# Optimization experiments

Hardware: AMD Instinct MI355X
Metric: run time of the kernel (lower is better)

## Reference

```python
import jax, jax.numpy as jnp
import numpy as np

B, N, C, H = 2, 2048, 1024, 16
D = C // H  # head_dim = 64

def setup_inputs() -> dict:
    key = jax.random.key(0)
    ks = jax.random.split(key, 8)
    x = jax.random.normal(ks[0], (B, N, C), jnp.float32)
    mask = jax.random.uniform(ks[1], (H, N, N), jnp.float32)
    gamma = jax.random.uniform(ks[2], (H,), jnp.float32)  # per-head decay in (0,1)
    state_prev = jax.random.normal(ks[3], (B, H, D, D), jnp.float32)
    w_scale = 0.02
    W_qkv = jax.random.normal(ks[4], (C, 3 * C), jnp.float32) * w_scale
    b_qkv = jnp.zeros((3 * C,), jnp.float32)
    W_out = jax.random.normal(ks[5], (C, C), jnp.float32) * w_scale
    b_out = jnp.zeros((C,), jnp.float32)
    return dict(x=x, mask=mask, gamma=gamma, state_prev=state_prev,
                W_qkv=W_qkv, b_qkv=b_qkv, W_out=W_out, b_out=b_out)

def reference(x, mask, gamma, state_prev, W_qkv, b_qkv, W_out, b_out):
    # Retention.chunkwise with state_prev (mode='chunkwise')
    b, n, c = x.shape
    h = gamma.shape[0]
    d = c // h
    scale = d ** -0.5
    qkv = (x @ W_qkv + b_qkv).reshape(b, n, 3, h, d)
    q = qkv[:, :, 0].transpose(0, 2, 1, 3) * scale  # [B,H,N,D]
    k = qkv[:, :, 1].transpose(0, 2, 1, 3)
    v = qkv[:, :, 2].transpose(0, 2, 1, 3)
    # intra-chunk decay-masked retention: [B,H,N,N]
    ret = jnp.einsum('bhnd,bhmd->bhnm', q, k) * mask
    ret = jnp.einsum('bhnm,bhmd->bhnd', ret, v)  # [B,H,N,D]
    inner_pos = jnp.arange(1, n + 1, dtype=x.dtype)  # [N], 1-based positions
    # state = sum_n gamma^(N-n) * k_n^T v_n (no [B,H,N,D,D] materialization)
    state_decays = gamma[:, None] ** (n - inner_pos)[None, :]  # [H,N]
    state = jnp.einsum('bhnd,bhne,hn->bhde', k, v, state_decays)  # [B,H,D,D]
    chunk_decay = gamma ** n  # [H]
    state = state + state_prev * chunk_decay[None, :, None, None]
    # cross-chunk retention against previous state
    cross = jnp.einsum('bhnd,bhde->bhne', q, state_prev)
    cross = cross * (gamma[None, :, None, None] ** inner_pos[None, None, :, None])
    ret = (ret + cross).transpose(0, 2, 1, 3).reshape(b, n, c)
    out = ret @ W_out + b_out
    return (out, state)
```

## Files before the change

### kernel.cpp

```cpp
#include <hip/hip_runtime.h>
#include <hip/hip_bf16.h>
#include <cstdint>

#define DI __device__ __forceinline__

typedef __attribute__((ext_vector_type(8))) short v8s;
typedef __attribute__((ext_vector_type(4))) float v4f;

constexpr int Bc = 2, Nc = 2048, Cc = 1024, Hc = 16, Dc = 64;

DI float bfbits(uint32_t u) { union { uint32_t i; float f; } c; c.i = u; return c.f; }
DI unsigned short f2bf(float f) {
    union { float f; uint32_t u; } c; c.f = f;
    uint32_t r = c.u + 0x7FFFu + ((c.u >> 16) & 1u);
    return (unsigned short)(r >> 16);
}
DI void unpackb8(uint4 u, float* f) {
    f[0] = bfbits(u.x << 16); f[1] = bfbits(u.x & 0xFFFF0000u);
    f[2] = bfbits(u.y << 16); f[3] = bfbits(u.y & 0xFFFF0000u);
    f[4] = bfbits(u.z << 16); f[5] = bfbits(u.z & 0xFFFF0000u);
    f[6] = bfbits(u.w << 16); f[7] = bfbits(u.w & 0xFFFF0000u);
}
DI float gpow(float g, float p) {
    if (p <= 0.f) return 1.f;
    if (g <= 0.f) return 0.f;
    return exp2f(p * log2f(g));
}

__global__ __launch_bounds__(256) void cvt_bf16(
    const float* __restrict__ in, unsigned short* __restrict__ out, int n8)
{
    int i = blockIdx.x * 256 + threadIdx.x;
    if (i >= n8) return;
    float4 a = ((const float4*)in)[i * 2];
    float4 b = ((const float4*)in)[i * 2 + 1];
    ushort4 r0; r0.x = f2bf(a.x); r0.y = f2bf(a.y); r0.z = f2bf(a.z); r0.w = f2bf(a.w);
    ushort4 r1; r1.x = f2bf(b.x); r1.y = f2bf(b.y); r1.z = f2bf(b.z); r1.w = f2bf(b.w);
    ((ushort4*)out)[i * 2] = r0; ((ushort4*)out)[i * 2 + 1] = r1;
}

__global__ __launch_bounds__(256) void transpose_cvt(
    const float* __restrict__ in, unsigned short* __restrict__ out, int R, int C)
{
    __shared__ float T[64][65];
    const int tid = threadIdx.x;
    const int r0 = blockIdx.y * 64, c0 = blockIdx.x * 64;
    #pragma unroll
    for (int rep = 0; rep < 4; rep++) {
        int row = (tid >> 4) + rep * 16, col = (tid & 15) * 4;
        float4 v = *reinterpret_cast<const float4*>(in + (size_t)(r0 + row) * C + c0 + col);
        T[row][col] = v.x; T[row][col + 1] = v.y; T[row][col + 2] = v.z; T[row][col + 3] = v.w;
    }
    __syncthreads();
    #pragma unroll
    for (int rep = 0; rep < 4; rep++) {
        int ocr = (tid >> 4) + rep * 16, j4 = (tid & 15) * 4;
        ushort4 w;
        w.x = f2bf(T[j4][ocr]);     w.y = f2bf(T[j4 + 1][ocr]);
        w.z = f2bf(T[j4 + 2][ocr]); w.w = f2bf(T[j4 + 3][ocr]);
        *reinterpret_cast<ushort4*>(out + (size_t)(c0 + ocr) * R + r0 + j4) = w;
    }
}

__global__ __launch_bounds__(256) void transpose_v(
    const unsigned short* __restrict__ in, unsigned short* __restrict__ out)
{
    __shared__ unsigned short T[64][72];
    const int tid = threadIdx.x;
    const int n0 = blockIdx.x * 64;
    const int bh = blockIdx.y;
    const unsigned short* src = in + ((size_t)bh * Nc + n0) * Dc;
    #pragma unroll
    for (int rep = 0; rep < 2; rep++) {
        int r = (tid >> 3) + rep * 32, c = (tid & 7) * 8;
        *(uint4*)&T[r][c] = *(const uint4*)(src + (size_t)r * Dc + c);
    }
    __syncthreads();
    unsigned short* dst = out + (size_t)bh * Dc * Nc + n0;
    #pragma unroll
    for (int rep = 0; rep < 2; rep++) {
        int d = (tid >> 3) + rep * 32, c0 = (tid & 7) * 8;
        union { uint4 u; unsigned short s[8]; } w;
        #pragma unroll
        for (int j = 0; j < 8; j++) w.s[j] = T[c0 + j][d];
        *(uint4*)(dst + (size_t)d * Nc + c0) = w.u;
    }
}

__global__ __launch_bounds__(256) void qkv_mfma(
    const unsigned short* __restrict__ A, const unsigned short* __restrict__ Bt,
    const float* __restrict__ bias,
    unsigned short* __restrict__ q, unsigned short* __restrict__ k,
    unsigned short* __restrict__ v)
{
    __shared__ unsigned short As[128][72];
    __shared__ unsigned short Bs[128][72];
    const int tid = threadIdx.x, wave = tid >> 6, lane = tid & 63;
    const int L = lane & 15, quad = lane >> 4;
    const int wr = (wave >> 1) * 64, wc = (wave & 1) * 64;
    const int row0 = blockIdx.y * 128, col0 = blockIdx.x * 128;
    v4f acc[4][4];
    #pragma unroll
    for (int i = 0; i < 4; i++)
        #pragma unroll
        for (int j = 0; j < 4; j++) { acc[i][j][0]=0.f; acc[i][j][1]=0.f; acc[i][j][2]=0.f; acc[i][j][3]=0.f; }
    for (int k0 = 0; k0 < 1024; k0 += 64) {
        __syncthreads();
        #pragma unroll
        for (int rep = 0; rep < 4; rep++) {
            int r = (tid >> 3) + rep * 32, cg = (tid & 7) * 8;
            *(uint4*)&As[r][cg] = *(const uint4*)(A  + (size_t)(row0 + r) * 1024 + k0 + cg);
            *(uint4*)&Bs[r][cg] = *(const uint4*)(Bt + (size_t)(col0 + r) * 1024 + k0 + cg);
        }
        __syncthreads();
        #pragma unroll
        for (int half = 0; half < 2; half++) {
            v8s af[4], bf[4];
            #pragma unroll
            for (int s = 0; s < 4; s++) {
                af[s] = *(v8s*)&As[wr + s * 16 + L][half * 32 + quad * 8];
                bf[s] = *(v8s*)&Bs[wc + s * 16 + L][half * 32 + quad * 8];
            }
            #pragma unroll
            for (int i = 0; i < 4; i++)
                #pragma unroll
                for (int j = 0; j < 4; j++)
                    acc[i][j] = __builtin_amdgcn_mfma_f32_16x16x32_bf16(af[i], bf[j], acc[i][j], 0, 0, 0);
        }
    }
    const int which = col0 >> 10;
    #pragma unroll
    for (int j = 0; j < 4; j++) {
        int c = col0 + wc + j * 16 + L;
        int h = (c & 1023) >> 6, d = c & 63;
        float bv = bias[c];
        #pragma unroll
        for (int i = 0; i < 4; i++) {
            #pragma unroll
            for (int reg = 0; reg < 4; reg++) {
                int rr = row0 + wr + i * 16 + quad * 4 + reg;
                int b = rr >> 11, n = rr & 2047;
                float val = acc[i][j][reg] + bv;
                size_t base = (((size_t)(b * Hc + h)) * Nc + n) * Dc + d;
                if (which == 0)      q[base] = f2bf(val * 0.125f);
                else if (which == 1) k[base] = f2bf(val);
                else                 v[base] = f2bf(val);
            }
        }
    }
}

__global__ __launch_bounds__(256) void retention_mfma(
    const unsigned short* __restrict__ qb, const unsigned short* __restrict__ kb,
    const unsigned short* __restrict__ vtb,
    const float* __restrict__ mask, const float* __restrict__ gamma,
    const float* __restrict__ sprev,
    unsigned short* __restrict__ retb, float* __restrict__ pf0, float* __restrict__ pf1)
{
    __shared__ unsigned short K0[64][72], K1[64][72];
    __shared__ unsigned short V0[64][72], V1[64][72];
    __shared__ unsigned short Sm[64][72];
    const int tid = threadIdx.x, wave = tid >> 6, lane = tid & 63;
    const int L = lane & 15, quad = lane >> 4;
    const int h = blockIdx.y;
    const int n0 = blockIdx.x * 64;
    const int chunk = blockIdx.z;
    const int m_base = chunk * 1024;
    const float g = gamma[h];
    const int bh0 = h, bh1 = Hc + h;

    {
        #pragma unroll
        for (int rep = 0; rep < 2; rep++) {
            int r = (tid >> 3) + rep * 32, ch = (tid & 7) * 8;
            *(uint4*)&V0[r][ch] = *(const uint4*)(qb + ((size_t)bh0 * Nc + n0 + r) * Dc + ch);
            *(uint4*)&V1[r][ch] = *(const uint4*)(qb + ((size_t)bh1 * Nc + n0 + r) * Dc + ch);
        }
        if (chunk == 0) {
            int dd = tid >> 2, e0 = (tid & 3) * 16;
            const float* sp0 = sprev + ((size_t)bh0 * 64 + dd) * 64 + e0;
            const float* sp1 = sprev + ((size_t)bh1 * 64 + dd) * 64 + e0;
            #pragma unroll
            for (int j = 0; j < 16; j++) K0[e0 + j][dd] = f2bf(sp0[j]);
            #pragma unroll
            for (int j = 0; j < 16; j++) K1[e0 + j][dd] = f2bf(sp1[j]);
        }
    }
    __syncthreads();
    v8s qf[2][2];
    qf[0][0] = *(v8s*)&V0[wave * 16 + L][quad * 8];
    qf[0][1] = *(v8s*)&V0[wave * 16 + L][32 + quad * 8];
    qf[1][0] = *(v8s*)&V1[wave * 16 + L][quad * 8];
    qf[1][1] = *(v8s*)&V1[wave * 16 + L][32 + quad * 8];
    v4f oacc[2][4];
    if (chunk == 0) {
        #pragma unroll
        for (int b = 0; b < 2; b++) {
            unsigned short (*Kb)[72] = b ? K1 : K0;
            #pragma unroll
            for (int s = 0; s < 4; s++) {
                v4f a; a[0] = 0.f; a[1] = 0.f; a[2] = 0.f; a[3] = 0.f;
                a = __builtin_amdgcn_mfma_f32_16x16x32_bf16(qf[b][0], *(v8s*)&Kb[s * 16 + L][quad * 8], a, 0, 0, 0);
                a = __builtin_amdgcn_mfma_f32_16x16x32_bf16(qf[b][1], *(v8s*)&Kb[s * 16 + L][32 + quad * 8], a, 0, 0, 0);
                oacc[b][s] = a;
            }
        }
        float cf = gpow(g, (float)(n0 + wave * 16 + quad * 4 + 1));
        #pragma unroll
        for (int reg = 0; reg < 4; reg++) {
            #pragma unroll
            for (int b = 0; b < 2; b++)
                #pragma unroll
                for (int s = 0; s < 4; s++) oacc[b][s][reg] *= cf;
            cf *= g;
        }
    } else {
        #pragma unroll
        for (int b = 0; b < 2; b++)
            #pragma unroll
            for (int s = 0; s < 4; s++) { oacc[b][s][0]=0.f; oacc[b][s][1]=0.f; oacc[b][s][2]=0.f; oacc[b][s][3]=0.f; }
    }

    const unsigned short* kp0 = kb + (size_t)bh0 * Nc * Dc;
    const unsigned short* kp1 = kb + (size_t)bh1 * Nc * Dc;
    const unsigned short* vt0 = vtb + (size_t)bh0 * Dc * Nc;
    const unsigned short* vt1 = vtb + (size_t)bh1 * Dc * Nc;
    const float* mbase = mask + (size_t)h * Nc * Nc;

    for (int it = 0; it < 16; ++it) {
        const int m0 = m_base + it * 64;
        __syncthreads();
        {
            #pragma unroll
            for (int rep = 0; rep < 2; rep++) {
                int r = (tid >> 3) + rep * 32, ch = (tid & 7) * 8;
                *(uint4*)&K0[r][ch] = *(const uint4*)(kp0 + (size_t)(m0 + r) * Dc + ch);
                *(uint4*)&K1[r][ch] = *(const uint4*)(kp1 + (size_t)(m0 + r) * Dc + ch);
                *(uint4*)&V0[r][ch] = *(const uint4*)(vt0 + (size_t)r * Nc + m0 + ch);
                *(uint4*)&V1[r][ch] = *(const uint4*)(vt1 + (size_t)r * Nc + m0 + ch);
            }
        }
        __syncthreads();
        float mv[4][4];
        #pragma unroll
        for (int s = 0; s < 4; s++)
            #pragma unroll
            for (int reg = 0; reg < 4; reg++)
                mv[s][reg] = mbase[(size_t)(n0 + wave * 16 + quad * 4 + reg) * Nc + m0 + s * 16 + L];
        #pragma unroll
        for (int b = 0; b < 2; b++) {
            unsigned short (*Kb)[72] = b ? K1 : K0;
            unsigned short (*Vb)[72] = b ? V1 : V0;
            v4f sa[4];
            #pragma unroll
            for (int s = 0; s < 4; s++) {
                v4f a; a[0] = 0.f; a[1] = 0.f; a[2] = 0.f; a[3] = 0.f;
                a = __builtin_amdgcn_mfma_f32_16x16x32_bf16(qf[b][0], *(v8s*)&Kb[s * 16 + L][quad * 8], a, 0, 0, 0);
                a = __builtin_amdgcn_mfma_f32_16x16x32_bf16(qf[b][1], *(v8s*)&Kb[s * 16 + L][32 + quad * 8], a, 0, 0, 0);
                sa[s] = a;
            }
            #pragma unroll
            for (int s = 0; s < 4; s++)
                #pragma unroll
                for (int reg = 0; reg < 4; reg++)
                    Sm[wave * 16 + quad * 4 + reg][s * 16 + L] = f2bf(sa[s][reg] * mv[s][reg]);
            v8s af0 = *(v8s*)&Sm[wave * 16 + L][quad * 8];
            v8s af1 = *(v8s*)&Sm[wave * 16 + L][32 + quad * 8];
            #pragma unroll
            for (int s = 0; s < 4; s++) {
                oacc[b][s] = __builtin_amdgcn_mfma_f32_16x16x32_bf16(af0, *(v8s*)&Vb[s * 16 + L][quad * 8], oacc[b][s], 0, 0, 0);
                oacc[b][s] = __builtin_amdgcn_mfma_f32_16x16x32_bf16(af1, *(v8s*)&Vb[s * 16 + L][32 + quad * 8], oacc[b][s], 0, 0, 0);
            }
        }
    }
    if (chunk == 0) {
        #pragma unroll
        for (int b = 0; b < 2; b++)
            #pragma unroll
            for (int s = 0; s < 4; s++)
                #pragma unroll
                for (int reg = 0; reg < 4; reg++) {
                    int n = n0 + wave * 16 + quad * 4 + reg;
                    retb[((size_t)b * Nc + n) * Cc + h * 64 + s * 16 + L] = f2bf(oacc[b][s][reg]);
                }
    } else {
        #pragma unroll
        for (int b = 0; b < 2; b++) {
            float* pd = b ? pf1 : pf0;
            #pragma unroll
            for (int s = 0; s < 4; s++)
                #pragma unroll
                for (int reg = 0; reg < 4; reg++) {
                    int n = n0 + wave * 16 + quad * 4 + reg;
                    pd[(size_t)n * Cc + h * 64 + s * 16 + L] = oacc[b][s][reg];
                }
        }
    }
}

__global__ __launch_bounds__(256) void add_partial(
    unsigned short* __restrict__ retb,
    const float* __restrict__ pf0, const float* __restrict__ pf1, int n8)
{
    int i = blockIdx.x * 256 + threadIdx.x;
    if (i >= n8) return;
    int e = i * 8;
    const float* pf = (e & (1 << 21)) ? pf1 : pf0;
    const float4* pp = (const float4*)(pf + (e & ((1 << 21) - 1)));
    uint4 a = ((const uint4*)retb)[i];
    float fa[8]; unpackb8(a, fa);
    float4 x0 = pp[0], x1 = pp[1];
    ushort4 r0, r1;
    r0.x = f2bf(fa[0] + x0.x); r0.y = f2bf(fa[1] + x0.y);
    r0.z = f2bf(fa[2] + x0.z); r0.w = f2bf(fa[3] + x0.w);
    r1.x = f2bf(fa[4] + x1.x); r1.y = f2bf(fa[5] + x1.y);
    r1.z = f2bf(fa[6] + x1.z); r1.w = f2bf(fa[7] + x1.w);
    ((ushort4*)retb)[2 * i] = r0; ((ushort4*)retb)[2 * i + 1] = r1;
}

__global__ __launch_bounds__(256) void state_partial(
    const unsigned short* __restrict__ kg, const unsigned short* __restrict__ vg,
    const float* __restrict__ gamma,
    float* __restrict__ partial)
{
    __shared__ float Ks[64][65];
    __shared__ float Vs[64][65];
    __shared__ float wdec[64];
    const int chunk = blockIdx.x;
    const int bh = blockIdx.y;
    const int h = bh & 15;
    const int tid = threadIdx.x;
    const int d = tid >> 2;
    const int e0 = (tid & 3) * 16;
    const float g = gamma[h];
    const unsigned short* kbp = kg + (size_t)bh * Nc * Dc;
    const unsigned short* vbp = vg + (size_t)bh * Nc * Dc;
    float acc[16] = {};
    const int nStart = chunk * 256;
    for (int m0 = nStart; m0 < nStart + 256; m0 += 64) {
        __syncthreads();
        {
            uint4 u0 = *(const uint4*)(kbp + (size_t)(m0 + d) * 64 + e0);
            uint4 u1 = *(const uint4*)(kbp + (size_t)(m0 + d) * 64 + e0 + 8);
            float f[8];
            unpackb8(u0, f);
            #pragma unroll
            for (int j = 0; j < 8; j++) Ks[d][e0 + j] = f[j];
            unpackb8(u1, f);
            #pragma unroll
            for (int j = 0; j < 8; j++) Ks[d][e0 + 8 + j] = f[j];
            uint4 w0 = *(const uint4*)(vbp + (size_t)(m0 + d) * 64 + e0);
            uint4 w1 = *(const uint4*)(vbp + (size_t)(m0 + d) * 64 + e0 + 8);
            unpackb8(w0, f);
            #pragma unroll
            for (int j = 0; j < 8; j++) Vs[d][e0 + j] = f[j];
            unpackb8(w1, f);
            #pragma unroll
            for (int j = 0; j < 8; j++) Vs[d][e0 + 8 + j] = f[j];
        }
        if (tid < 64) wdec[tid] = gpow(g, (float)(2047 - (m0 + tid)));
        __syncthreads();
        for (int nn = 0; nn < 64; nn++) {
            float kw = Ks[nn][d] * wdec[nn];
            #pragma unroll
            for (int j = 0; j < 16; j++) acc[j] += kw * Vs[nn][e0 + j];
        }
    }
    float* pp = partial + (size_t)chunk * (Bc * Hc * Dc * Dc)
              + ((size_t)bh * 64 + d) * 64 + e0;
    #pragma unroll
    for (int j = 0; j < 16; j++) pp[j] = acc[j];
}

__global__ __launch_bounds__(256) void state_reduce(
    const float* __restrict__ partial,
    const float* __restrict__ sprev,
    const float* __restrict__ gamma,
    float* __restrict__ outState)
{
    const int idx = blockIdx.x * 256 + threadIdx.x;
    const int bh = idx >> 12;
    const int h = bh & 15;
    const float g = gamma[h];
    float acc = sprev[idx] * gpow(g, 2048.f);
    #pragma unroll
    for (int c = 0; c < 8; c++) acc += partial[(size_t)c * (Bc * Hc * Dc * Dc) + idx];
    outState[idx] = acc;
}

__global__ __launch_bounds__(256) void out_mfma(
    const unsigned short* __restrict__ A, const unsigned short* __restrict__ Bt,
    const float* __restrict__ bias,
    float* __restrict__ out)
{
    __shared__ unsigned short As[128][72];
    __shared__ unsigned short Bs[128][72];
    const int tid = threadIdx.x, wave = tid >> 6, lane = tid & 63;
    const int L = lane & 15, quad = lane >> 4;
    const int wr = (wave >> 1) * 64, wc = (wave & 1) * 64;
    const int row0 = blockIdx.y * 128, col0 = blockIdx.x * 128;
    v4f acc[4][4];
    #pragma unroll
    for (int i = 0; i < 4; i++)
        #pragma unroll
        for (int j = 0; j < 4; j++) { acc[i][j][0]=0.f; acc[i][j][1]=0.f; acc[i][j][2]=0.f; acc[i][j][3]=0.f; }
    for (int k0 = 0; k0 < 1024; k0 += 64) {
        __syncthreads();
        #pragma unroll
        for (int rep = 0; rep < 4; rep++) {
            int r = (tid >> 3) + rep * 32, cg = (tid & 7) * 8;
            *(uint4*)&As[r][cg] = *(const uint4*)(A  + (size_t)(row0 + r) * 1024 + k0 + cg);
            *(uint4*)&Bs[r][cg] = *(const uint4*)(Bt + (size_t)(col0 + r) * 1024 + k0 + cg);
        }
        __syncthreads();
        #pragma unroll
        for (int half = 0; half < 2; half++) {
            v8s af[4], bf[4];
            #pragma unroll
            for (int s = 0; s < 4; s++) {
                af[s] = *(v8s*)&As[wr + s * 16 + L][half * 32 + quad * 8];
                bf[s] = *(v8s*)&Bs[wc + s * 16 + L][half * 32 + quad * 8];
            }
            #pragma unroll
            for (int i = 0; i < 4; i++)
                #pragma unroll
                for (int j = 0; j < 4; j++)
                    acc[i][j] = __builtin_amdgcn_mfma_f32_16x16x32_bf16(af[i], bf[j], acc[i][j], 0, 0, 0);
        }
    }
    #pragma unroll
    for (int j = 0; j < 4; j++) {
        int c = col0 + wc + j * 16 + L;
        float bv = bias[c];
        #pragma unroll
        for (int i = 0; i < 4; i++) {
            #pragma unroll
            for (int reg = 0; reg < 4; reg++) {
                int rr = row0 + wr + i * 16 + quad * 4 + reg;
                out[(size_t)rr * 1024 + c] = acc[i][j][reg] + bv;
            }
        }
    }
}

extern "C" void kernel_launch(void* const* d_in, const int* in_sizes, int n_in,
                              void* d_out, int out_size, void* d_ws, size_t ws_size,
                              hipStream_t stream) {
    (void)in_sizes; (void)n_in; (void)out_size; (void)ws_size;
    const float* x     = (const float*)d_in[0];
    const float* mask  = (const float*)d_in[1];
    const float* gamma = (const float*)d_in[2];
    const float* sprev = (const float*)d_in[3];
    const float* Wqkv  = (const float*)d_in[4];
    const float* bqkv  = (const float*)d_in[5];
    const float* Wout  = (const float*)d_in[6];
    const float* bout  = (const float*)d_in[7];

    char* W = (char*)d_ws;
    unsigned short* qb   = (unsigned short*)(W);
    unsigned short* kb   = (unsigned short*)(W + 8388608);
    unsigned short* vb   = (unsigned short*)(W + 16777216);
    float*          pf0  = (float*)        (W + 16777216);
    unsigned short* retb = (unsigned short*)(W + 25165824);
    unsigned short* wot  = (unsigned short*)(W + 33554432);
    float*          part = (float*)        (W + 35651584);
    unsigned short* xb   = (unsigned short*)(W + 39845888);
    unsigned short* vtb  = (unsigned short*)(W + 39845888);
    unsigned short* wqt  = (unsigned short*)(W + 48234496);
    float*          pf1  = (float*)        (W + 54525952);

    float* out      = (float*)d_out;
    float* outState = (float*)d_out + (size_t)Bc * Nc * Cc;

    cvt_bf16<<<2048, 256, 0, stream>>>(x, xb, 524288);
    transpose_cvt<<<dim3(48, 16), 256, 0, stream>>>(Wqkv, wqt, 1024, 3072);
    transpose_cvt<<<dim3(16, 16), 256, 0, stream>>>(Wout, wot, 1024, 1024);
    qkv_mfma<<<dim3(24, 32), 256, 0, stream>>>(xb, wqt, bqkv, qb, kb, vb);
    transpose_v<<<dim3(32, 32), 256, 0, stream>>>(vb, vtb);
    state_partial<<<dim3(8, 32), 256, 0, stream>>>(kb, vb, gamma, part);
    state_reduce<<<512, 256, 0, stream>>>(part, sprev, gamma, outState);
    retention_mfma<<<dim3(32, 16, 2), 256, 0, stream>>>(qb, kb, vtb, mask, gamma, sprev,
                                                        retb, pf0, pf1);
    add_partial<<<2048, 256, 0, stream>>>(retb, pf0, pf1, 524288);
    out_mfma<<<dim3(8, 32), 256, 0, stream>>>(retb, wot, bout, out);
}
```

Before: 604.0 us.

## Retile retention kernel to 128 query rows per block for a single batch

```diff
diff --git a/kernel.cpp b/kernel.cpp
--- a/kernel.cpp
+++ b/kernel.cpp
@@ -150,113 +150,105 @@
     }
 }
 
-__global__ __launch_bounds__(256) void retention_mfma(
+__global__ __launch_bounds__(256, 4) void retention_mfma(
     const unsigned short* __restrict__ qb, const unsigned short* __restrict__ kb,
     const unsigned short* __restrict__ vtb,
     const float* __restrict__ mask, const float* __restrict__ gamma,
     const float* __restrict__ sprev,
     unsigned short* __restrict__ retb, float* __restrict__ pf0, float* __restrict__ pf1)
 {
-    __shared__ unsigned short K0[64][72], K1[64][72];
-    __shared__ unsigned short V0[64][72], V1[64][72];
+    __shared__ unsigned short Kt[64][72];
+    __shared__ unsigned short Vt[64][72];
     __shared__ unsigned short Sm[64][72];
     const int tid = threadIdx.x, wave = tid >> 6, lane = tid & 63;
     const int L = lane & 15, quad = lane >> 4;
     const int h = blockIdx.y;
-    const int n0 = blockIdx.x * 64;
-    const int chunk = blockIdx.z;
+    const int n0 = blockIdx.x * 128;
+    const int batch = blockIdx.z >> 1;
+    const int chunk = blockIdx.z & 1;
     const int m_base = chunk * 1024;
     const float g = gamma[h];
-    const int bh0 = h, bh1 = Hc + h;
+    const int bh = batch * Hc + h;
 
     {
         #pragma unroll
         for (int rep = 0; rep < 2; rep++) {
             int r = (tid >> 3) + rep * 32, ch = (tid & 7) * 8;
-            *(uint4*)&V0[r][ch] = *(const uint4*)(qb + ((size_t)bh0 * Nc + n0 + r) * Dc + ch);
-            *(uint4*)&V1[r][ch] = *(const uint4*)(qb + ((size_t)bh1 * Nc + n0 + r) * Dc + ch);
-        }
-        if (chunk == 0) {
-            int dd = tid >> 2, e0 = (tid & 3) * 16;
-            const float* sp0 = sprev + ((size_t)bh0 * 64 + dd) * 64 + e0;
-            const float* sp1 = sprev + ((size_t)bh1 * 64 + dd) * 64 + e0;
-            #pragma unroll
-            for (int j = 0; j < 16; j++) K0[e0 + j][dd] = f2bf(sp0[j]);
-            #pragma unroll
-            for (int j = 0; j < 16; j++) K1[e0 + j][dd] = f2bf(sp1[j]);
+            *(uint4*)&Kt[r][ch] = *(const uint4*)(qb + ((size_t)bh * Nc + n0 + r) * Dc + ch);
+            *(uint4*)&Vt[r][ch] = *(const uint4*)(qb + ((size_t)bh * Nc + n0 + 64 + r) * Dc + ch);
         }
     }
     __syncthreads();
     v8s qf[2][2];
-    qf[0][0] = *(v8s*)&V0[wave * 16 + L][quad * 8];
-    qf[0][1] = *(v8s*)&V0[wave * 16 + L][32 + quad * 8];
-    qf[1][0] = *(v8s*)&V1[wave * 16 + L][quad * 8];
-    qf[1][1] = *(v8s*)&V1[wave * 16 + L][32 + quad * 8];
+    qf[0][0] = *(v8s*)&Kt[wave * 16 + L][quad * 8];
+    qf[0][1] = *(v8s*)&Kt[wave * 16 + L][32 + quad * 8];
+    qf[1][0] = *(v8s*)&Vt[wave * 16 + L][quad * 8];
+    qf[1][1] = *(v8s*)&Vt[wave * 16 + L][32 + quad * 8];
+
     v4f oacc[2][4];
+    #pragma unroll
+    for (int band = 0; band < 2; band++)
+        #pragma unroll
+        for (int s = 0; s < 4; s++) { oacc[band][s][0]=0.f; oacc[band][s][1]=0.f; oacc[band][s][2]=0.f; oacc[band][s][3]=0.f; }
+
     if (chunk == 0) {
-        #pragma unroll
-        for (int b = 0; b < 2; b++) {
-            unsigned short (*Kb)[72] = b ? K1 : K0;
+        __syncthreads();
+        {
+            int dd = tid >> 2, e0 = (tid & 3) * 16;
+            const float* sp = sprev + ((size_t)bh * 64 + dd) * 64 + e0;
+            #pragma unroll
+            for (int j = 0; j < 16; j++) Kt[e0 + j][dd] = f2bf(sp[j]);
+        }
+        __syncthreads();
+        #pragma unroll
+        for (int band = 0; band < 2; band++) {
+            #pragma unroll
+            for (int s = 0; s < 4; s++) {
+                v4f a = oacc[band][s];
+                a = __builtin_amdgcn_mfma_f32_16x16x32_bf16(qf[band][0], *(v8s*)&Kt[s * 16 + L][quad * 8], a, 0, 0, 0);
+                a = __builtin_amdgcn_mfma_f32_16x16x32_bf16(qf[band][1], *(v8s*)&Kt[s * 16 + L][32 + quad * 8], a, 0, 0, 0);
+                oacc[band][s] = a;
+            }
+            float cf = gpow(g, (float)(n0 + band * 64 + wave * 16 + quad * 4 + 1));
+            #pragma unroll
+            for (int reg = 0; reg < 4; reg++) {
+                #pragma unroll
+                for (int s = 0; s < 4; s++) oacc[band][s][reg] *= cf;
+                cf *= g;
+            }
+        }
+    }
+
+    const unsigned short* kp = kb + (size_t)bh * Nc * Dc;
+    const unsigned short* vt = vtb + (size_t)bh * Dc * Nc;
+    const float* mbase = mask + (size_t)h * Nc * Nc;
+
+    for (int it = 0; it < 16; ++it) {
+        const int m0 = m_base + it * 64;
+        __syncthreads();
+        {
+            #pragma unroll
+            for (int rep = 0; rep < 2; rep++) {
+                int r = (tid >> 3) + rep * 32, ch = (tid & 7) * 8;
+                *(uint4*)&Kt[r][ch] = *(const uint4*)(kp + (size_t)(m0 + r) * Dc + ch);
+                *(uint4*)&Vt[r][ch] = *(const uint4*)(vt + (size_t)r * Nc + m0 + ch);
+            }
+        }
+        __syncthreads();
+        #pragma unroll
+        for (int band = 0; band < 2; band++) {
+            float mv[4][4];
+            #pragma unroll
+            for (int s = 0; s < 4; s++)
+                #pragma unroll
+                for (int reg = 0; reg < 4; reg++)
+                    mv[s][reg] = mbase[(size_t)(n0 + band * 64 + wave * 16 + quad * 4 + reg) * Nc + m0 + s * 16 + L];
+            v4f sa[4];
             #pragma unroll
             for (int s = 0; s < 4; s++) {
                 v4f a; a[0] = 0.f; a[1] = 0.f; a[2] = 0.f; a[3] = 0.f;
-                a = __builtin_amdgcn_mfma_f32_16x16x32_bf16(qf[b][0], *(v8s*)&Kb[s * 16 + L][quad * 8], a, 0, 0, 0);
-                a = __builtin_amdgcn_mfma_f32_16x16x32_bf16(qf[b][1], *(v8s*)&Kb[s * 16 + L][32 + quad * 8], a, 0, 0, 0);
-                oacc[b][s] = a;
-            }
-        }
-        float cf = gpow(g, (float)(n0 + wave * 16 + quad * 4 + 1));
-        #pragma unroll
-        for (int reg = 0; reg < 4; reg++) {
-            #pragma unroll
-            for (int b = 0; b < 2; b++)
-                #pragma unroll
-                for (int s = 0; s < 4; s++) oacc[b][s][reg] *= cf;
-            cf *= g;
-        }
-    } else {
-        #pragma unroll
-        for (int b = 0; b < 2; b++)
-            #pragma unroll
-            for (int s = 0; s < 4; s++) { oacc[b][s][0]=0.f; oacc[b][s][1]=0.f; oacc[b][s][2]=0.f; oacc[b][s][3]=0.f; }
-    }
-
-    const unsigned short* kp0 = kb + (size_t)bh0 * Nc * Dc;
-    const unsigned short* kp1 = kb + (size_t)bh1 * Nc * Dc;
-    const unsigned short* vt0 = vtb + (size_t)bh0 * Dc * Nc;
-    const unsigned short* vt1 = vtb + (size_t)bh1 * Dc * Nc;
-    const float* mbase = mask + (size_t)h * Nc * Nc;
-
-    for (int it = 0; it < 16; ++it) {
-        const int m0 = m_base + it * 64;
-        __syncthreads();
-        {
-            #pragma unroll
-            for (int rep = 0; rep < 2; rep++) {
-                int r = (tid >> 3) + rep * 32, ch = (tid & 7) * 8;
-                *(uint4*)&K0[r][ch] = *(const uint4*)(kp0 + (size_t)(m0 + r) * Dc + ch);
-                *(uint4*)&K1[r][ch] = *(const uint4*)(kp1 + (size_t)(m0 + r) * Dc + ch);
-                *(uint4*)&V0[r][ch] = *(const uint4*)(vt0 + (size_t)r * Nc + m0 + ch);
-                *(uint4*)&V1[r][ch] = *(const uint4*)(vt1 + (size_t)r * Nc + m0 + ch);
-            }
-        }
-        __syncthreads();
-        float mv[4][4];
-        #pragma unroll
-        for (int s = 0; s < 4; s++)
-            #pragma unroll
-            for (int reg = 0; reg < 4; reg++)
-                mv[s][reg] = mbase[(size_t)(n0 + wave * 16 + quad * 4 + reg) * Nc + m0 + s * 16 + L];
-        #pragma unroll
-        for (int b = 0; b < 2; b++) {
-            unsigned short (*Kb)[72] = b ? K1 : K0;
-            unsigned short (*Vb)[72] = b ? V1 : V0;
-            v4f sa[4];
-            #pragma unroll
-            for (int s = 0; s < 4; s++) {
-                v4f a; a[0] = 0.f; a[1] = 0.f; a[2] = 0.f; a[3] = 0.f;
-                a = __builtin_amdgcn_mfma_f32_16x16x32_bf16(qf[b][0], *(v8s*)&Kb[s * 16 + L][quad * 8], a, 0, 0, 0);
-                a = __builtin_amdgcn_mfma_f32_16x16x32_bf16(qf[b][1], *(v8s*)&Kb[s * 16 + L][32 + quad * 8], a, 0, 0, 0);
+                a = __builtin_amdgcn_mfma_f32_16x16x32_bf16(qf[band][0], *(v8s*)&Kt[s * 16 + L][quad * 8], a, 0, 0, 0);
+                a = __builtin_amdgcn_mfma_f32_16x16x32_bf16(qf[band][1], *(v8s*)&Kt[s * 16 + L][32 + quad * 8], a, 0, 0, 0);
                 sa[s] = a;
             }
             #pragma unroll
@@ -268,33 +260,33 @@
             v8s af1 = *(v8s*)&Sm[wave * 16 + L][32 + quad * 8];
             #pragma unroll
             for (int s = 0; s < 4; s++) {
-                oacc[b][s] = __builtin_amdgcn_mfma_f32_16x16x32_bf16(af0, *(v8s*)&Vb[s * 16 + L][quad * 8], oacc[b][s], 0, 0, 0);
-                oacc[b][s] = __builtin_amdgcn_mfma_f32_16x16x32_bf16(af1, *(v8s*)&Vb[s * 16 + L][32 + quad * 8], oacc[b][s], 0, 0, 0);
-            }
-        }
-    }
+                oacc[band][s] = __builtin_amdgcn_mfma_f32_16x16x32_bf16(af0, *(v8s*)&Vt[s * 16 + L][quad * 8], oacc[band][s], 0, 0, 0);
+                oacc[band][s] = __builtin_amdgcn_mfma_f32_16x16x32_bf16(af1, *(v8s*)&Vt[s * 16 + L][32 + quad * 8], oacc[band][s], 0, 0, 0);
+            }
+        }
+    }
+
     if (chunk == 0) {
         #pragma unroll
-        for (int b = 0; b < 2; b++)
+        for (int band = 0; band < 2; band++)
             #pragma unroll
             for (int s = 0; s < 4; s++)
                 #pragma unroll
                 for (int reg = 0; reg < 4; reg++) {
-                    int n = n0 + wave * 16 + quad * 4 + reg;
-                    retb[((size_t)b * Nc + n) * Cc + h * 64 + s * 16 + L] = f2bf(oacc[b][s][reg]);
+                    int n = n0 + band * 64 + wave * 16 + quad * 4 + reg;
+                    retb[((size_t)batch * Nc + n) * Cc + h * 64 + s * 16 + L] = f2bf(oacc[band][s][reg]);
                 }
     } else {
-        #pragma unroll
-        for (int b = 0; b < 2; b++) {
-            float* pd = b ? pf1 : pf0;
+        float* pd = batch ? pf1 : pf0;
+        #pragma unroll
+        for (int band = 0; band < 2; band++)
             #pragma unroll
             for (int s = 0; s < 4; s++)
                 #pragma unroll
                 for (int reg = 0; reg < 4; reg++) {
-                    int n = n0 + wave * 16 + quad * 4 + reg;
-                    pd[(size_t)n * Cc + h * 64 + s * 16 + L] = oacc[b][s][reg];
+                    int n = n0 + band * 64 + wave * 16 + quad * 4 + reg;
+                    pd[(size_t)n * Cc + h * 64 + s * 16 + L] = oacc[band][s][reg];
                 }
-        }
     }
 }
 
@@ -479,7 +471,7 @@
     transpose_v<<<dim3(32, 32), 256, 0, stream>>>(vb, vtb);
     state_partial<<<dim3(8, 32), 256, 0, stream>>>(kb, vb, gamma, part);
     state_reduce<<<512, 256, 0, stream>>>(part, sprev, gamma, outState);
-    retention_mfma<<<dim3(32, 16, 2), 256, 0, stream>>>(qb, kb, vtb, mask, gamma, sprev,
+    retention_mfma<<<dim3(16, 16, 4), 256, 0, stream>>>(qb, kb, vtb, mask, gamma, sprev,
                                                         retb, pf0, pf1);
     add_partial<<<2048, 256, 0, stream>>>(retb, pf0, pf1, 524288);
     out_mfma<<<dim3(8, 32), 256, 0, stream>>>(retb, wot, bout, out);
```

Result: faster. 551.4 us (-8.7%).
